# Performance work log

Measured on AMD Instinct MI355X. Metric: run time of the kernel, lower is better.

The kernel has to match this reference:

```python
import jax, jax.numpy as jnp
import numpy as np

N_NODES = 100000
N_EDGES = 1600000


def setup_inputs() -> dict:
    key = jax.random.key(0)
    ks = jax.random.split(key, 5)
    x = jax.random.normal(ks[0], (N_NODES, 128), dtype=jnp.float32)
    edge_index = jax.random.randint(ks[1], (2, N_EDGES), 0, N_NODES, dtype=jnp.int64)
    edge_weight = jnp.ones((N_EDGES,), dtype=jnp.float32)
    W1 = jax.random.normal(ks[2], (128, 128), dtype=jnp.float32) * (1.0 / np.sqrt(128))
    b1 = jnp.zeros((128,), dtype=jnp.float32)
    W2 = jax.random.normal(ks[3], (128, 64), dtype=jnp.float32) * (1.0 / np.sqrt(128))
    b2 = jnp.zeros((64,), dtype=jnp.float32)
    return {"x": x, "edge_index": edge_index, "edge_weight": edge_weight,
            "W1": W1, "b1": b1, "W2": W2, "b2": b2}


def _gcn_conv(x, rows, cols, W, b, n_nodes):
    # GCNConv(normalize=True), unit edge weights (forward overwrites weights with ones)
    h = x @ W                                             # [N, out]
    ones_w = jnp.ones(rows.shape[0], dtype=x.dtype)
    deg = jax.ops.segment_sum(ones_w, cols, num_segments=n_nodes)   # in-degree at targets
    dinv = jnp.where(deg > 0, deg ** -0.5, 0.0)
    norm = dinv[rows] * dinv[cols]                        # [E+N]
    msg = h[rows] * norm[:, None]                         # gather + scale, memory-bound
    out = jax.ops.segment_sum(msg, cols, num_segments=n_nodes)
    return out + b


def reference(x, edge_index, edge_weight, W1, b1, W2, b2):
    n = x.shape[0]
    loop = jnp.arange(n, dtype=edge_index.dtype)
    rows = jnp.concatenate([edge_index[0], loop])         # self-loops (PyG default)
    cols = jnp.concatenate([edge_index[1], loop])
    h = jax.nn.relu(_gcn_conv(x, rows, cols, W1, b1, n))
    logits = _gcn_conv(h, rows, cols, W2, b2, n)
    return logits
```

## Files before the change

kernel.cpp:

```cpp
#include <hip/hip_runtime.h>
#include <hip/hip_fp16.h>


constexpr int NN = 100000;
constexpr int NE = 1600000;
constexpr int BSH = 7;
constexpr int NB = (NN + 127) >> BSH;
constexpr int NBLK = 256;
constexpr int EPB = NE / NBLK;
constexpr int TSTR = 784;

typedef _Float16 f16x8 __attribute__((ext_vector_type(8)));
typedef float f32x4 __attribute__((ext_vector_type(4)));

__global__ __launch_bounds__(256) void k_hist(const int* __restrict__ cols,
                                              int* __restrict__ table) {
  __shared__ int cnt[NB];
  for (int i = threadIdx.x; i < NB; i += 256) cnt[i] = 0;
  __syncthreads();
  int base = blockIdx.x * EPB;
  for (int i = threadIdx.x; i < EPB; i += 256)
    atomicAdd(&cnt[cols[base + i] >> BSH], 1);
  __syncthreads();
  for (int i = threadIdx.x; i < NB; i += 256)
    table[blockIdx.x * TSTR + i] = cnt[i];
}

__global__ __launch_bounds__(256) void k_scanT(const int* __restrict__ table,
                                               int* __restrict__ startOff,
                                               int* __restrict__ btot) {
  __shared__ int s[256];
  int b = blockIdx.x, t = threadIdx.x;
  int v = table[t * TSTR + b];
  s[t] = v;
  __syncthreads();
  for (int off = 1; off < 256; off <<= 1) {
    int tmp = (t >= off) ? s[t - off] : 0;
    __syncthreads();
    s[t] += tmp;
    __syncthreads();
  }
  startOff[t * TSTR + b] = s[t] - v;
  if (t == 255) btot[b] = s[t];
}

__global__ __launch_bounds__(256) void k_scanBkt(const int* __restrict__ btot,
                                                 int* __restrict__ bucketBase) {
  __shared__ int s[256];
  int t = threadIdx.x;
  int base = t * 4;
  int d0 = (base + 0 < NB) ? btot[base + 0] : 0;
  int d1 = (base + 1 < NB) ? btot[base + 1] : 0;
  int d2 = (base + 2 < NB) ? btot[base + 2] : 0;
  int d3 = (base + 3 < NB) ? btot[base + 3] : 0;
  int tsum = d0 + d1 + d2 + d3;
  s[t] = tsum;
  __syncthreads();
  for (int off = 1; off < 256; off <<= 1) {
    int tmp = (t >= off) ? s[t - off] : 0;
    __syncthreads();
    s[t] += tmp;
    __syncthreads();
  }
  int ex = s[t] - tsum;
  if (base + 0 < NB) bucketBase[base + 0] = ex;
  if (base + 1 < NB) bucketBase[base + 1] = ex + d0;
  if (base + 2 < NB) bucketBase[base + 2] = ex + d0 + d1;
  if (base + 3 < NB) bucketBase[base + 3] = ex + d0 + d1 + d2;
}

__global__ __launch_bounds__(256) void k_scat(const int* __restrict__ rows,
                                              const int* __restrict__ cols,
                                              const int* __restrict__ startOff,
                                              const int* __restrict__ bucketBase,
                                              unsigned* __restrict__ binned) {
  __shared__ int scnt[NB];
  int blk = blockIdx.x;
  for (int i = threadIdx.x; i < NB; i += 256)
    scnt[i] = bucketBase[i] + startOff[blk * TSTR + i];
  __syncthreads();
  int base = blk * EPB;
  for (int i = threadIdx.x; i < EPB; i += 256) {
    int c = cols[base + i];
    int r = rows[base + i];
    int pos = atomicAdd(&scnt[c >> BSH], 1);
    binned[pos] = ((unsigned)r << BSH) | (unsigned)(c & 127);
  }
}

__global__ __launch_bounds__(256) void k_fillb(const unsigned* __restrict__ binned,
                                               const int* __restrict__ bucketBase,
                                               const int* __restrict__ btot,
                                               int* __restrict__ rowptr,
                                               int* __restrict__ deg,
                                               float* __restrict__ dinv,
                                               int* __restrict__ srcIdx) {
  __shared__ int cnt[128];
  __shared__ int sc[128];
  __shared__ int rp[128];
  int b = blockIdx.x;
  int nb0 = b << BSH;
  int nn = min(128, NN - nb0);
  int tid = threadIdx.x;
  if (tid < 128) cnt[tid] = 0;
  __syncthreads();
  int ebeg = bucketBase[b];
  int eend = ebeg + btot[b];
  for (int p = ebeg + tid; p < eend; p += 256)
    atomicAdd(&cnt[binned[p] & 127], 1);
  __syncthreads();
  int v = (tid < 128) ? cnt[tid] : 0;
  if (tid < 128) sc[tid] = v;
  __syncthreads();
  for (int off = 1; off < 128; off <<= 1) {
    int tmp = (tid < 128 && tid >= off) ? sc[tid - off] : 0;
    __syncthreads();
    if (tid < 128) sc[tid] += tmp;
    __syncthreads();
  }
  if (tid < 128) {
    int ex = sc[tid] - v;
    rp[tid] = ebeg + ex;
    if (tid < nn) {
      rowptr[nb0 + tid] = ebeg + ex;
      deg[nb0 + tid] = v;
      dinv[nb0 + tid] = rsqrtf((float)v + 1.0f);
    }
    cnt[tid] = 0;
  }
  __syncthreads();
  for (int p = ebeg + tid; p < eend; p += 256) {
    unsigned pk = binned[p];
    int cl = pk & 127;
    int local = atomicAdd(&cnt[cl], 1);
    srcIdx[rp[cl] + local] = (int)(pk >> BSH);
  }
}

__global__ __launch_bounds__(256) void k_wt(const float* __restrict__ W,
                                            __half* __restrict__ Wt, int K, int N) {
  int i = blockIdx.x * 256 + threadIdx.x;
  if (i < K * N) {
    int k = i / N, n = i % N;
    Wt[n * K + k] = __float2half(W[i]);
  }
}

__global__ __launch_bounds__(256) void k_y(const float4* __restrict__ x4,
                                           const float* __restrict__ dinv,
                                           float2* __restrict__ y8) {
  int gid = blockIdx.x * 256 + threadIdx.x;
  if (gid >= NN * 32) return;
  float s = dinv[gid >> 5];
  float4 v = x4[gid];
  union { __half2 h[2]; float2 f; } u;
  u.h[0] = __floats2half2_rn(v.x * s, v.y * s);
  u.h[1] = __floats2half2_rn(v.z * s, v.w * s);
  y8[gid] = u.f;
}

__global__ __launch_bounds__(256) void k_gath1(const __half* __restrict__ y,
                                               const int* __restrict__ rowptr,
                                               const int* __restrict__ deg,
                                               const int* __restrict__ srcIdx,
                                               const float* __restrict__ dinv,
                                               __half* __restrict__ agg) {
  int node = blockIdx.x * 4 + (threadIdx.x >> 6);
  if (node >= NN) return;
  int lane = threadIdx.x & 63;
  int g = lane >> 4;
  int c = lane & 15;
  int d = deg[node];
  int p = rowptr[node];
  size_t coff = (size_t)c * 8;
  float acc[8];
#pragma unroll
  for (int i = 0; i < 8; i++) acc[i] = 0.0f;

  for (int base = 0; base < d; base += 64) {
    int cnt = min(64, d - base);
    int my = (lane < cnt) ? srcIdx[p + base + lane] : 0;
    int k = 0;
    for (; k + 8 <= cnt; k += 8) {
      int s0 = __shfl(my, k + g);
      int s1 = __shfl(my, k + 4 + g);
      f16x8 v0 = *reinterpret_cast<const f16x8*>(y + (size_t)s0 * 128 + coff);
      f16x8 v1 = *reinterpret_cast<const f16x8*>(y + (size_t)s1 * 128 + coff);
#pragma unroll
      for (int i = 0; i < 8; i++) acc[i] += (float)v0[i];
#pragma unroll
      for (int i = 0; i < 8; i++) acc[i] += (float)v1[i];
    }
    for (; k < cnt; k += 4) {
      int idx = k + g;
      bool valid = idx < cnt;
      int s0 = __shfl(my, valid ? idx : 0);
      f16x8 v0 = *reinterpret_cast<const f16x8*>(y + (size_t)s0 * 128 + coff);
      if (valid) {
#pragma unroll
        for (int i = 0; i < 8; i++) acc[i] += (float)v0[i];
      }
    }
  }
#pragma unroll
  for (int i = 0; i < 8; i++) acc[i] += __shfl_xor(acc[i], 16);
#pragma unroll
  for (int i = 0; i < 8; i++) acc[i] += __shfl_xor(acc[i], 32);
  if (g == 0) {
    f16x8 sv = *reinterpret_cast<const f16x8*>(y + (size_t)node * 128 + coff);
    float sc = dinv[node];
    union { __half2 h[4]; float4 f; } o;
#pragma unroll
    for (int j = 0; j < 4; j++) {
      float a = (acc[2 * j]     + (float)sv[2 * j])     * sc;
      float b = (acc[2 * j + 1] + (float)sv[2 * j + 1]) * sc;
      o.h[j] = __floats2half2_rn(a, b);
    }
    *reinterpret_cast<float4*>(agg + (size_t)node * 128 + coff) = o.f;
  }
}

__global__ __launch_bounds__(256) void k_gath2(const __half* __restrict__ z,
                                               const int* __restrict__ rowptr,
                                               const int* __restrict__ deg,
                                               const int* __restrict__ srcIdx,
                                               const float* __restrict__ dinv,
                                               const float* __restrict__ b2,
                                               float* __restrict__ out) {
  int node = blockIdx.x * 4 + (threadIdx.x >> 6);
  if (node >= NN) return;
  int lane = threadIdx.x & 63;
  int g = lane >> 3;
  int c = lane & 7;
  int d = deg[node];
  int p = rowptr[node];
  size_t coff = (size_t)c * 8;
  float acc[8];
#pragma unroll
  for (int i = 0; i < 8; i++) acc[i] = 0.0f;

  for (int base = 0; base < d; base += 64) {
    int cnt = min(64, d - base);
    int my = (lane < cnt) ? srcIdx[p + base + lane] : 0;
    int k = 0;
    for (; k + 16 <= cnt; k += 16) {
      int s0 = __shfl(my, k + g);
      int s1 = __shfl(my, k + 8 + g);
      f16x8 v0 = *reinterpret_cast<const f16x8*>(z + (size_t)s0 * 64 + coff);
      f16x8 v1 = *reinterpret_cast<const f16x8*>(z + (size_t)s1 * 64 + coff);
#pragma unroll
      for (int i = 0; i < 8; i++) acc[i] += (float)v0[i];
#pragma unroll
      for (int i = 0; i < 8; i++) acc[i] += (float)v1[i];
    }
    for (; k < cnt; k += 8) {
      int idx = k + g;
      bool valid = idx < cnt;
      int s0 = __shfl(my, valid ? idx : 0);
      f16x8 v0 = *reinterpret_cast<const f16x8*>(z + (size_t)s0 * 64 + coff);
      if (valid) {
#pragma unroll
        for (int i = 0; i < 8; i++) acc[i] += (float)v0[i];
      }
    }
  }
#pragma unroll
  for (int i = 0; i < 8; i++) acc[i] += __shfl_xor(acc[i], 8);
#pragma unroll
  for (int i = 0; i < 8; i++) acc[i] += __shfl_xor(acc[i], 16);
#pragma unroll
  for (int i = 0; i < 8; i++) acc[i] += __shfl_xor(acc[i], 32);
  if (g == 0) {
    f16x8 sv = *reinterpret_cast<const f16x8*>(z + (size_t)node * 64 + coff);
    float s = dinv[node];
    const float4* b4 = reinterpret_cast<const float4*>(b2);
    float4 bv0 = b4[2 * c], bv1 = b4[2 * c + 1];
    float4 o0, o1;
    o0.x = (acc[0] + (float)sv[0]) * s + bv0.x;
    o0.y = (acc[1] + (float)sv[1]) * s + bv0.y;
    o0.z = (acc[2] + (float)sv[2]) * s + bv0.z;
    o0.w = (acc[3] + (float)sv[3]) * s + bv0.w;
    o1.x = (acc[4] + (float)sv[4]) * s + bv1.x;
    o1.y = (acc[5] + (float)sv[5]) * s + bv1.y;
    o1.z = (acc[6] + (float)sv[6]) * s + bv1.z;
    o1.w = (acc[7] + (float)sv[7]) * s + bv1.w;
    float4* op = reinterpret_cast<float4*>(out + (size_t)node * 64 + coff);
    op[0] = o0;
    op[1] = o1;
  }
}

template <int BN, bool BIASRELU, bool ROWSCALE>
__global__ __launch_bounds__(256) void k_gemmM(const __half* __restrict__ A,
                                               const __half* __restrict__ Wt,
                                               const float* __restrict__ bias,
                                               const float* __restrict__ rowscale,
                                               __half* __restrict__ C, int M) {
  constexpr int NT = BN / 16;
  __shared__ __half tile[4][16][BN + 8];
  const int w = threadIdx.x >> 6, l = threadIdx.x & 63;
  const int quad = l >> 4, m = l & 15;
  const int rowTop = blockIdx.x * 64 + w * 16;

  f32x4 acc[NT];
#pragma unroll
  for (int t = 0; t < NT; t++) {
    float bv = BIASRELU ? bias[t * 16 + m] : 0.0f;
    acc[t] = (f32x4){bv, bv, bv, bv};
  }

  int arow = rowTop + m;
  if (arow >= M) arow = M - 1;
  const __half* ap = A + (size_t)arow * 128 + quad * 8;

#pragma unroll
  for (int kc = 0; kc < 128; kc += 32) {
    f16x8 a = *reinterpret_cast<const f16x8*>(ap + kc);
#pragma unroll
    for (int t = 0; t < NT; t++) {
      f16x8 b = *reinterpret_cast<const f16x8*>(
          Wt + (size_t)(t * 16 + m) * 128 + kc + quad * 8);
      acc[t] = __builtin_amdgcn_mfma_f32_16x16x32_f16(a, b, acc[t], 0, 0, 0);
    }
  }

  float rs[4];
  if constexpr (ROWSCALE) {
#pragma unroll
    for (int i = 0; i < 4; i++) {
      int r = rowTop + quad * 4 + i;
      rs[i] = rowscale[r < M ? r : M - 1];
    }
  }
#pragma unroll
  for (int t = 0; t < NT; t++)
#pragma unroll
    for (int i = 0; i < 4; i++) {
      float v = acc[t][i];
      if constexpr (BIASRELU) v = fmaxf(v, 0.0f);
      if constexpr (ROWSCALE) v *= rs[i];
      tile[w][quad * 4 + i][t * 16 + m] = __float2half(v);
    }
  __syncthreads();

  constexpr int CH = 16 * BN / 8;
#pragma unroll
  for (int rep = 0; rep < CH / 64; rep++) {
    int idx = rep * 64 + l;
    int r = idx / (BN / 8), cc = idx % (BN / 8);
    int grow = rowTop + r;
    if (grow < M)
      *reinterpret_cast<float4*>(C + (size_t)grow * BN + cc * 8) =
          *reinterpret_cast<const float4*>(&tile[w][r][cc * 8]);
  }
}

extern "C" void kernel_launch(void* const* d_in, const int* in_sizes, int n_in,
                              void* d_out, int out_size, void* d_ws, size_t ws_size,
                              hipStream_t stream) {
  const float* x  = (const float*)d_in[0];
  const int*   ei = (const int*)d_in[1];
  const int* rows = ei;
  const int* cols = ei + NE;
  const float* W1 = (const float*)d_in[3];
  const float* b1 = (const float*)d_in[4];
  const float* W2 = (const float*)d_in[5];
  const float* b2 = (const float*)d_in[6];
  float* out = (float*)d_out;

  char* base = (char*)d_ws;
  constexpr size_t MB = 1 << 20;
  int*      deg       = (int*)(base + 0 * MB);
  int*      rowptr    = (int*)(base + 1 * MB);
  float*    dinv      = (float*)(base + 2 * MB);
  int*      btot      = (int*)(base + 3 * MB);
  int*      bucketBase= (int*)(base + 3 * MB + 16 * 1024);
  __half*   Wt1       = (__half*)(base + 3 * MB + 64 * 1024);
  __half*   Wt2       = (__half*)(base + 3 * MB + 128 * 1024);
  int*      table     = (int*)(base + 4 * MB);
  int*      startOff  = (int*)(base + 5 * MB);
  unsigned* binned    = (unsigned*)(base + 6 * MB);
  int*      srcIdx    = (int*)(base + 13 * MB);
  __half*   y         = (__half*)(base + 20 * MB);
  __half*   aggx      = (__half*)(base + 46 * MB);
  __half*   h1        = (__half*)(base + 72 * MB);
  __half*   z         = (__half*)(base + 20 * MB);

  k_wt<<<64, 256, 0, stream>>>(W1, Wt1, 128, 128);
  k_wt<<<32, 256, 0, stream>>>(W2, Wt2, 128, 64);
  k_hist<<<NBLK, 256, 0, stream>>>(cols, table);
  k_scanT<<<NB, 256, 0, stream>>>(table, startOff, btot);
  k_scanBkt<<<1, 256, 0, stream>>>(btot, bucketBase);
  k_scat<<<NBLK, 256, 0, stream>>>(rows, cols, startOff, bucketBase, binned);
  k_fillb<<<NB, 256, 0, stream>>>(binned, bucketBase, btot, rowptr, deg, dinv,
                                  srcIdx);
  k_y<<<(NN * 32 + 255) / 256, 256, 0, stream>>>((const float4*)x, dinv, (float2*)y);
  k_gath1<<<(NN + 3) / 4, 256, 0, stream>>>(y, rowptr, deg, srcIdx, dinv, aggx);
  k_gemmM<128, true, false><<<(NN + 63) / 64, 256, 0, stream>>>(
      aggx, Wt1, b1, nullptr, h1, NN);
  k_gemmM<64, false, true><<<(NN + 63) / 64, 256, 0, stream>>>(
      h1, Wt2, nullptr, dinv, z, NN);
  k_gath2<<<(NN + 3) / 4, 256, 0, stream>>>(z, rowptr, deg, srcIdx, dinv, b2, out);
}
```

Baseline: 328.7 us.

## Fuse layer-1 gather with both GEMMs and fold x scaling into CSR build

The layer-1 neighbour aggregation, the W1 GEMM with bias and ReLU, and the W2 GEMM with row scaling now run in one kernel. Each wave gathers 16 nodes into shared memory and feeds them straight into MFMA, so the aggx and h1 intermediates no longer go through global memory. The dinv-scaled fp16 conversion of x moves into k_fillb, and the two weight transposes share one launch, removing several launches. The trade-off is fewer lanes per node in the gather (16 instead of 64) and a single sequential kernel doing gather plus GEMM, which may expose latency. There is also no bounds guard on the last partial tile (NN is a multiple of 16, so this happens to work).

```diff
diff --git a/kernel.cpp b/kernel.cpp
--- a/kernel.cpp
+++ b/kernel.cpp
@@ -94,10 +94,13 @@
                                                int* __restrict__ rowptr,
                                                int* __restrict__ deg,
                                                float* __restrict__ dinv,
-                                               int* __restrict__ srcIdx) {
+                                               int* __restrict__ srcIdx,
+                                               const float4* __restrict__ x4,
+                                               float2* __restrict__ y8) {
   __shared__ int cnt[128];
   __shared__ int sc[128];
   __shared__ int rp[128];
+  __shared__ float sdv[128];
   int b = blockIdx.x;
   int nb0 = b << BSH;
   int nn = min(128, NN - nb0);
@@ -121,10 +124,12 @@
   if (tid < 128) {
     int ex = sc[tid] - v;
     rp[tid] = ebeg + ex;
+    float dv = rsqrtf((float)v + 1.0f);
+    sdv[tid] = dv;
     if (tid < nn) {
       rowptr[nb0 + tid] = ebeg + ex;
       deg[nb0 + tid] = v;
-      dinv[nb0 + tid] = rsqrtf((float)v + 1.0f);
+      dinv[nb0 + tid] = dv;
     }
     cnt[tid] = 0;
   }
@@ -135,88 +140,134 @@
     int local = atomicAdd(&cnt[cl], 1);
     srcIdx[rp[cl] + local] = (int)(pk >> BSH);
   }
-}
-
-__global__ __launch_bounds__(256) void k_wt(const float* __restrict__ W,
-                                            __half* __restrict__ Wt, int K, int N) {
+  int tot = nn << 5;
+  const float4* xb = x4 + ((size_t)nb0 << 5);
+  float2* yb = y8 + ((size_t)nb0 << 5);
+  for (int i = tid; i < tot; i += 256) {
+    float s = sdv[i >> 5];
+    float4 vv = xb[i];
+    union { __half2 h[2]; float2 f; } u;
+    u.h[0] = __floats2half2_rn(vv.x * s, vv.y * s);
+    u.h[1] = __floats2half2_rn(vv.z * s, vv.w * s);
+    yb[i] = u.f;
+  }
+}
+
+__global__ __launch_bounds__(256) void k_wt(const float* __restrict__ W1,
+                                            const float* __restrict__ W2,
+                                            __half* __restrict__ Wt1,
+                                            __half* __restrict__ Wt2) {
   int i = blockIdx.x * 256 + threadIdx.x;
-  if (i < K * N) {
-    int k = i / N, n = i % N;
-    Wt[n * K + k] = __float2half(W[i]);
-  }
-}
-
-__global__ __launch_bounds__(256) void k_y(const float4* __restrict__ x4,
-                                           const float* __restrict__ dinv,
-                                           float2* __restrict__ y8) {
-  int gid = blockIdx.x * 256 + threadIdx.x;
-  if (gid >= NN * 32) return;
-  float s = dinv[gid >> 5];
-  float4 v = x4[gid];
-  union { __half2 h[2]; float2 f; } u;
-  u.h[0] = __floats2half2_rn(v.x * s, v.y * s);
-  u.h[1] = __floats2half2_rn(v.z * s, v.w * s);
-  y8[gid] = u.f;
-}
-
-__global__ __launch_bounds__(256) void k_gath1(const __half* __restrict__ y,
-                                               const int* __restrict__ rowptr,
-                                               const int* __restrict__ deg,
-                                               const int* __restrict__ srcIdx,
-                                               const float* __restrict__ dinv,
-                                               __half* __restrict__ agg) {
-  int node = blockIdx.x * 4 + (threadIdx.x >> 6);
-  if (node >= NN) return;
-  int lane = threadIdx.x & 63;
-  int g = lane >> 4;
-  int c = lane & 15;
-  int d = deg[node];
-  int p = rowptr[node];
-  size_t coff = (size_t)c * 8;
-  float acc[8];
-#pragma unroll
-  for (int i = 0; i < 8; i++) acc[i] = 0.0f;
-
-  for (int base = 0; base < d; base += 64) {
-    int cnt = min(64, d - base);
-    int my = (lane < cnt) ? srcIdx[p + base + lane] : 0;
-    int k = 0;
-    for (; k + 8 <= cnt; k += 8) {
-      int s0 = __shfl(my, k + g);
-      int s1 = __shfl(my, k + 4 + g);
-      f16x8 v0 = *reinterpret_cast<const f16x8*>(y + (size_t)s0 * 128 + coff);
-      f16x8 v1 = *reinterpret_cast<const f16x8*>(y + (size_t)s1 * 128 + coff);
-#pragma unroll
-      for (int i = 0; i < 8; i++) acc[i] += (float)v0[i];
-#pragma unroll
-      for (int i = 0; i < 8; i++) acc[i] += (float)v1[i];
-    }
-    for (; k < cnt; k += 4) {
-      int idx = k + g;
-      bool valid = idx < cnt;
-      int s0 = __shfl(my, valid ? idx : 0);
-      f16x8 v0 = *reinterpret_cast<const f16x8*>(y + (size_t)s0 * 128 + coff);
-      if (valid) {
+  if (i < 16384) {
+    int k = i >> 7, n = i & 127;
+    Wt1[n * 128 + k] = __float2half(W1[i]);
+  } else {
+    int j = i - 16384;
+    int k = j >> 6, n = j & 63;
+    Wt2[n * 128 + k] = __float2half(W2[j]);
+  }
+}
+
+__global__ __launch_bounds__(256) void k_fused(
+    const __half* __restrict__ y, const int* __restrict__ rowptr,
+    const int* __restrict__ deg, const int* __restrict__ srcIdx,
+    const float* __restrict__ dinv, const __half* __restrict__ Wt1,
+    const float* __restrict__ b1, const __half* __restrict__ Wt2,
+    __half* __restrict__ z) {
+  __shared__ __align__(16) __half sA[4][16][136];
+  __shared__ __align__(16) __half sB[4][16][136];
+  const int w = threadIdx.x >> 6, l = threadIdx.x & 63;
+  const int rowTop = blockIdx.x * 64 + w * 16;
+  if (rowTop >= NN) return;
+  const int quad = l >> 4, m = l & 15;
+  const int sb = l & 48;
+
+  for (int p = 0; p < 4; ++p) {
+    int node = rowTop + p * 4 + quad;
+    int d = deg[node];
+    int ptr = rowptr[node];
+    float acc[8];
+#pragma unroll
+    for (int i = 0; i < 8; i++) acc[i] = 0.0f;
+    for (int base = 0; base < d; base += 16) {
+      int cntv = min(16, d - base);
+      int my = (m < cntv) ? srcIdx[ptr + base + m] : 0;
+      int k = 0;
+      for (; k + 2 <= cntv; k += 2) {
+        int s0 = __shfl(my, sb + k);
+        int s1 = __shfl(my, sb + k + 1);
+        f16x8 v0 = *reinterpret_cast<const f16x8*>(y + (size_t)s0 * 128 + m * 8);
+        f16x8 v1 = *reinterpret_cast<const f16x8*>(y + (size_t)s1 * 128 + m * 8);
+#pragma unroll
+        for (int i = 0; i < 8; i++) acc[i] += (float)v0[i];
+#pragma unroll
+        for (int i = 0; i < 8; i++) acc[i] += (float)v1[i];
+      }
+      if (k < cntv) {
+        int s0 = __shfl(my, sb + k);
+        f16x8 v0 = *reinterpret_cast<const f16x8*>(y + (size_t)s0 * 128 + m * 8);
 #pragma unroll
         for (int i = 0; i < 8; i++) acc[i] += (float)v0[i];
       }
     }
-  }
-#pragma unroll
-  for (int i = 0; i < 8; i++) acc[i] += __shfl_xor(acc[i], 16);
-#pragma unroll
-  for (int i = 0; i < 8; i++) acc[i] += __shfl_xor(acc[i], 32);
-  if (g == 0) {
-    f16x8 sv = *reinterpret_cast<const f16x8*>(y + (size_t)node * 128 + coff);
-    float sc = dinv[node];
-    union { __half2 h[4]; float4 f; } o;
-#pragma unroll
-    for (int j = 0; j < 4; j++) {
-      float a = (acc[2 * j]     + (float)sv[2 * j])     * sc;
-      float b = (acc[2 * j + 1] + (float)sv[2 * j + 1]) * sc;
-      o.h[j] = __floats2half2_rn(a, b);
-    }
-    *reinterpret_cast<float4*>(agg + (size_t)node * 128 + coff) = o.f;
+    f16x8 sv = *reinterpret_cast<const f16x8*>(y + (size_t)node * 128 + m * 8);
+    float scn = dinv[node];
+    f16x8 o;
+#pragma unroll
+    for (int i = 0; i < 8; i++) o[i] = (_Float16)((acc[i] + (float)sv[i]) * scn);
+    *reinterpret_cast<f16x8*>(&sA[w][p * 4 + quad][m * 8]) = o;
+  }
+
+  f32x4 acc1[8];
+#pragma unroll
+  for (int t = 0; t < 8; t++) {
+    float bv = b1[t * 16 + m];
+    acc1[t] = (f32x4){bv, bv, bv, bv};
+  }
+#pragma unroll
+  for (int kc = 0; kc < 128; kc += 32) {
+    f16x8 a = *reinterpret_cast<const f16x8*>(&sA[w][m][kc + quad * 8]);
+#pragma unroll
+    for (int t = 0; t < 8; t++) {
+      f16x8 b = *reinterpret_cast<const f16x8*>(
+          Wt1 + (size_t)(t * 16 + m) * 128 + kc + quad * 8);
+      acc1[t] = __builtin_amdgcn_mfma_f32_16x16x32_f16(a, b, acc1[t], 0, 0, 0);
+    }
+  }
+#pragma unroll
+  for (int t = 0; t < 8; t++)
+#pragma unroll
+    for (int i = 0; i < 4; i++)
+      sB[w][quad * 4 + i][t * 16 + m] = __float2half(fmaxf(acc1[t][i], 0.0f));
+
+  f32x4 acc2[4];
+#pragma unroll
+  for (int t = 0; t < 4; t++) acc2[t] = (f32x4){0.f, 0.f, 0.f, 0.f};
+#pragma unroll
+  for (int kc = 0; kc < 128; kc += 32) {
+    f16x8 a = *reinterpret_cast<const f16x8*>(&sB[w][m][kc + quad * 8]);
+#pragma unroll
+    for (int t = 0; t < 4; t++) {
+      f16x8 b = *reinterpret_cast<const f16x8*>(
+          Wt2 + (size_t)(t * 16 + m) * 128 + kc + quad * 8);
+      acc2[t] = __builtin_amdgcn_mfma_f32_16x16x32_f16(a, b, acc2[t], 0, 0, 0);
+    }
+  }
+  float rs[4];
+#pragma unroll
+  for (int i = 0; i < 4; i++) rs[i] = dinv[rowTop + quad * 4 + i];
+#pragma unroll
+  for (int t = 0; t < 4; t++)
+#pragma unroll
+    for (int i = 0; i < 4; i++)
+      sA[w][quad * 4 + i][t * 16 + m] = __float2half(acc2[t][i] * rs[i]);
+
+#pragma unroll
+  for (int rep = 0; rep < 2; rep++) {
+    int idx = rep * 64 + l;
+    int r = idx >> 3, cc = idx & 7;
+    *reinterpret_cast<float4*>(z + (size_t)(rowTop + r) * 64 + cc * 8) =
+        *reinterpret_cast<const float4*>(&sA[w][r][cc * 8]);
   }
 }
 
@@ -290,71 +341,6 @@
   }
 }
 
-template <int BN, bool BIASRELU, bool ROWSCALE>
-__global__ __launch_bounds__(256) void k_gemmM(const __half* __restrict__ A,
-                                               const __half* __restrict__ Wt,
-                                               const float* __restrict__ bias,
-                                               const float* __restrict__ rowscale,
-                                               __half* __restrict__ C, int M) {
-  constexpr int NT = BN / 16;
-  __shared__ __half tile[4][16][BN + 8];
-  const int w = threadIdx.x >> 6, l = threadIdx.x & 63;
-  const int quad = l >> 4, m = l & 15;
-  const int rowTop = blockIdx.x * 64 + w * 16;
-
-  f32x4 acc[NT];
-#pragma unroll
-  for (int t = 0; t < NT; t++) {
-    float bv = BIASRELU ? bias[t * 16 + m] : 0.0f;
-    acc[t] = (f32x4){bv, bv, bv, bv};
-  }
-
-  int arow = rowTop + m;
-  if (arow >= M) arow = M - 1;
-  const __half* ap = A + (size_t)arow * 128 + quad * 8;
-
-#pragma unroll
-  for (int kc = 0; kc < 128; kc += 32) {
-    f16x8 a = *reinterpret_cast<const f16x8*>(ap + kc);
-#pragma unroll
-    for (int t = 0; t < NT; t++) {
-      f16x8 b = *reinterpret_cast<const f16x8*>(
-          Wt + (size_t)(t * 16 + m) * 128 + kc + quad * 8);
-      acc[t] = __builtin_amdgcn_mfma_f32_16x16x32_f16(a, b, acc[t], 0, 0, 0);
-    }
-  }
-
-  float rs[4];
-  if constexpr (ROWSCALE) {
-#pragma unroll
-    for (int i = 0; i < 4; i++) {
-      int r = rowTop + quad * 4 + i;
-      rs[i] = rowscale[r < M ? r : M - 1];
-    }
-  }
-#pragma unroll
-  for (int t = 0; t < NT; t++)
-#pragma unroll
-    for (int i = 0; i < 4; i++) {
-      float v = acc[t][i];
-      if constexpr (BIASRELU) v = fmaxf(v, 0.0f);
-      if constexpr (ROWSCALE) v *= rs[i];
-      tile[w][quad * 4 + i][t * 16 + m] = __float2half(v);
-    }
-  __syncthreads();
-
-  constexpr int CH = 16 * BN / 8;
-#pragma unroll
-  for (int rep = 0; rep < CH / 64; rep++) {
-    int idx = rep * 64 + l;
-    int r = idx / (BN / 8), cc = idx % (BN / 8);
-    int grow = rowTop + r;
-    if (grow < M)
-      *reinterpret_cast<float4*>(C + (size_t)grow * BN + cc * 8) =
-          *reinterpret_cast<const float4*>(&tile[w][r][cc * 8]);
-  }
-}
-
 extern "C" void kernel_launch(void* const* d_in, const int* in_sizes, int n_in,
                               void* d_out, int out_size, void* d_ws, size_t ws_size,
                               hipStream_t stream) {
@@ -382,23 +368,16 @@
   unsigned* binned    = (unsigned*)(base + 6 * MB);
   int*      srcIdx    = (int*)(base + 13 * MB);
   __half*   y         = (__half*)(base + 20 * MB);
-  __half*   aggx      = (__half*)(base + 46 * MB);
-  __half*   h1        = (__half*)(base + 72 * MB);
-  __half*   z         = (__half*)(base + 20 * MB);
-
-  k_wt<<<64, 256, 0, stream>>>(W1, Wt1, 128, 128);
-  k_wt<<<32, 256, 0, stream>>>(W2, Wt2, 128, 64);
+  __half*   z         = (__half*)(base + 46 * MB);
+
+  k_wt<<<96, 256, 0, stream>>>(W1, W2, Wt1, Wt2);
   k_hist<<<NBLK, 256, 0, stream>>>(cols, table);
   k_scanT<<<NB, 256, 0, stream>>>(table, startOff, btot);
   k_scanBkt<<<1, 256, 0, stream>>>(btot, bucketBase);
   k_scat<<<NBLK, 256, 0, stream>>>(rows, cols, startOff, bucketBase, binned);
   k_fillb<<<NB, 256, 0, stream>>>(binned, bucketBase, btot, rowptr, deg, dinv,
-                                  srcIdx);
-  k_y<<<(NN * 32 + 255) / 256, 256, 0, stream>>>((const float4*)x, dinv, (float2*)y);
-  k_gath1<<<(NN + 3) / 4, 256, 0, stream>>>(y, rowptr, deg, srcIdx, dinv, aggx);
-  k_gemmM<128, true, false><<<(NN + 63) / 64, 256, 0, stream>>>(
-      aggx, Wt1, b1, nullptr, h1, NN);
-  k_gemmM<64, false, true><<<(NN + 63) / 64, 256, 0, stream>>>(
-      h1, Wt2, nullptr, dinv, z, NN);
+                                  srcIdx, (const float4*)x, (float2*)y);
+  k_fused<<<(NN + 63) / 64, 256, 0, stream>>>(y, rowptr, deg, srcIdx, dinv,
+                                              Wt1, b1, Wt2, z);
   k_gath2<<<(NN + 3) / 4, 256, 0, stream>>>(z, rowptr, deg, srcIdx, dinv, b2, out);
 }
```

Result: faster. 317.1 us (-3.5%).
